# Kernel tuning notes

Measured on AMD Instinct MI355X. Metric: run time of the kernel, lower is better.

## Reference

```python
import jax, jax.numpy as jnp
import numpy as np
import math

H = 1024      # d_input / d_output channels
N = 64        # d_state (diagonal SSM size)
L = 2048      # kernel / sequence length
DT_MIN, DT_MAX = 0.001, 0.1
HIGH_STAB, LOW_STAB = -0.9, -0.8


def setup_inputs() -> dict:
    key = jax.random.key(0)
    k1, k2, k3, k4 = jax.random.split(key, 4)
    # log_dt ~ U[log(dt_min), log(dt_max)]
    log_dt = jax.random.uniform(k1, (H,), dtype=jnp.float32) \
        * (math.log(DT_MAX) - math.log(DT_MIN)) + math.log(DT_MIN)
    # C ~ complex normal, stored as real pairs (H, N, 2) like torch.view_as_real
    C = jax.random.normal(k2, (H, N, 2), dtype=jnp.float32)
    # Diagonal A: Re(A) uniform in [high_stability, low_stability] (stable),
    # Im(A) random; stored as real pairs (N, 2). A is a frozen buffer.
    a_re = jax.random.uniform(k3, (N,), dtype=jnp.float32) * (LOW_STAB - HIGH_STAB) + HIGH_STAB
    a_im = jax.random.normal(k4, (N,), dtype=jnp.float32) * math.pi
    A = jnp.stack([a_re, a_im], axis=-1)
    return {"log_dt": log_dt, "C": C, "A": A, "input_length": L}


def reference(log_dt, C, A, input_length):
    # log_dt: (H,) float32; C: (H,N,2) float32; A: (N,2) float32
    dt = jnp.exp(log_dt)                                   # (H,)
    Cc = (C[..., 0] + 1j * C[..., 1]).astype(jnp.complex64)  # (H, N)
    Ac = (A[..., 0] + 1j * A[..., 1]).astype(jnp.complex64)  # (N,)
    dtA = dt[:, None].astype(jnp.complex64) * Ac[None, :]  # (H, N)
    # Vandermonde-style kernel: exp(dtA * l) for l in [0, L)
    l = jnp.arange(input_length, dtype=jnp.float32).astype(jnp.complex64)  # (L,)
    Kexp = jnp.exp(dtA[:, :, None] * l[None, None, :])     # (H, N, L) complex64
    Cmod = Cc * (jnp.exp(dtA) - 1.0) / Ac                  # (H, N)
    K = 2.0 * jnp.einsum('hn,hnl->hl', Cmod, Kexp).real    # (H, L) float32
    return K
```

## Files before the change

### kernel.cpp

```cpp
#include <hip/hip_runtime.h>

#define H 1024
#define N 64
#define L 2048
#define TPB 256
#define KK (L / TPB)

#define INV2PI 0.15915494309189535f

__device__ __forceinline__ float fexp(float x) {
    return __expf(x);
}

__global__ void s4d_precomp(const float* __restrict__ log_dt,
                            const float* __restrict__ Cv,
                            const float* __restrict__ Av,
                            float4* __restrict__ P1,
                            float2* __restrict__ P2)
{
    int idx = blockIdx.x * blockDim.x + threadIdx.x;
    if (idx >= H * N) return;
    int h = idx >> 6;
    int n = idx & (N - 1);

    float dt = fexp(log_dt[h]);
    float ar = Av[2 * n], ai = Av[2 * n + 1];
    float dr = dt * ar, di = dt * ai;

    float mr  = fexp(dr);
    float rev = di * INV2PI;
    rev -= floorf(rev);
    float rr = mr * __builtin_amdgcn_cosf(rev);
    float ri = mr * __builtin_amdgcn_sinf(rev);

    float ms   = fexp(dr * (float)TPB);
    float revs = di * ((float)TPB * INV2PI);
    revs -= floorf(revs);
    float sr = ms * __builtin_amdgcn_cosf(revs);
    float si = ms * __builtin_amdgcn_sinf(revs);

    float cr = Cv[2 * idx], ci = Cv[2 * idx + 1];
    float er = rr - 1.0f, ei = ri;
    float tr = cr * er - ci * ei;
    float ti = cr * ei + ci * er;
    float inv = 2.0f / (ar * ar + ai * ai);
    float cmr = (tr * ar + ti * ai) * inv;
    float cmi = (ti * ar - tr * ai) * inv;

    P1[idx] = make_float4(dr, di, sr, si);
    P2[idx] = make_float2(cmr, cmi);
}

__global__ __launch_bounds__(TPB) void s4d_main(const float4* __restrict__ P1,
                                                const float2* __restrict__ P2,
                                                float* __restrict__ out)
{
    __shared__ float4 l1[N];
    __shared__ float2 l2[N];

    const int h = blockIdx.x;
    const int t = threadIdx.x;
    if (t < N) {
        l1[t] = P1[h * N + t];
        l2[t] = P2[h * N + t];
    }
    __syncthreads();

    float acc[KK];
#pragma unroll
    for (int k = 0; k < KK; ++k) acc[k] = 0.0f;

    const float tf = (float)t;

#pragma unroll 2
    for (int n = 0; n < N; ++n) {
        float4 a = l1[n];
        float2 c = l2[n];

        float m   = fexp(a.x * tf);
        float rev = (a.y * tf) * INV2PI;
        rev -= floorf(rev);
        float cs = __builtin_amdgcn_cosf(rev);
        float sn = __builtin_amdgcn_sinf(rev);
        float wre = m * (c.x * cs - c.y * sn);
        float wim = m * (c.x * sn + c.y * cs);

#pragma unroll
        for (int k = 0; k < KK; ++k) {
            acc[k] += wre;
            float nr = wre * a.z - wim * a.w;
            wim      = wre * a.w + wim * a.z;
            wre      = nr;
        }
    }

    float* o = out + h * L + t;
#pragma unroll
    for (int k = 0; k < KK; ++k) o[k * TPB] = acc[k];
}

extern "C" void kernel_launch(void* const* d_in, const int* in_sizes, int n_in,
                              void* d_out, int out_size, void* d_ws, size_t ws_size,
                              hipStream_t stream) {
    const float* log_dt = (const float*)d_in[0];
    const float* Cv     = (const float*)d_in[1];
    const float* Av     = (const float*)d_in[2];
    float* out          = (float*)d_out;

    float4* P1 = (float4*)d_ws;
    float2* P2 = (float2*)((char*)d_ws + (size_t)H * N * sizeof(float4));

    s4d_precomp<<<(H * N + 255) / 256, 256, 0, stream>>>(log_dt, Cv, Av, P1, P2);
    s4d_main<<<H, TPB, 0, stream>>>(P1, P2, out);
}
```

Measured before the change: 87.78 us.

## Fuse precompute into main kernel and use packed FP32 complex math

The separate precompute kernel is folded into the main kernel: the first 64 threads of each block compute the per-(h,n) decay, step and C-modulation terms directly into shared memory, which removes one launch and the workspace round trip. The inner complex recurrence now uses inline-asm v_pk_mul_f32/v_pk_fma_f32 and v_pk_add_f32 on two-wide float vectors, aiming to halve the VALU instruction count of the complex multiply-accumulate. The accumulator also carries an unused imaginary lane, which doubles accumulator registers and packed-add work. The 2π scaling is folded into the stored phase to save a multiply per step.

```diff
diff --git a/kernel.cpp b/kernel.cpp
--- a/kernel.cpp
+++ b/kernel.cpp
@@ -8,95 +8,99 @@
 
 #define INV2PI 0.15915494309189535f
 
-__device__ __forceinline__ float fexp(float x) {
-    return __expf(x);
+typedef float f32x2 __attribute__((ext_vector_type(2)));
+
+
+__device__ __forceinline__ f32x2 pk_add(f32x2 a, f32x2 b) {
+    f32x2 d;
+    asm("v_pk_add_f32 %0, %1, %2" : "=v"(d) : "v"(a), "v"(b));
+    return d;
 }
 
-__global__ void s4d_precomp(const float* __restrict__ log_dt,
-                            const float* __restrict__ Cv,
-                            const float* __restrict__ Av,
-                            float4* __restrict__ P1,
-                            float2* __restrict__ P2)
-{
-    int idx = blockIdx.x * blockDim.x + threadIdx.x;
-    if (idx >= H * N) return;
-    int h = idx >> 6;
-    int n = idx & (N - 1);
-
-    float dt = fexp(log_dt[h]);
-    float ar = Av[2 * n], ai = Av[2 * n + 1];
-    float dr = dt * ar, di = dt * ai;
-
-    float mr  = fexp(dr);
-    float rev = di * INV2PI;
-    rev -= floorf(rev);
-    float rr = mr * __builtin_amdgcn_cosf(rev);
-    float ri = mr * __builtin_amdgcn_sinf(rev);
-
-    float ms   = fexp(dr * (float)TPB);
-    float revs = di * ((float)TPB * INV2PI);
-    revs -= floorf(revs);
-    float sr = ms * __builtin_amdgcn_cosf(revs);
-    float si = ms * __builtin_amdgcn_sinf(revs);
-
-    float cr = Cv[2 * idx], ci = Cv[2 * idx + 1];
-    float er = rr - 1.0f, ei = ri;
-    float tr = cr * er - ci * ei;
-    float ti = cr * ei + ci * er;
-    float inv = 2.0f / (ar * ar + ai * ai);
-    float cmr = (tr * ar + ti * ai) * inv;
-    float cmi = (ti * ar - tr * ai) * inv;
-
-    P1[idx] = make_float4(dr, di, sr, si);
-    P2[idx] = make_float2(cmr, cmi);
+__device__ __forceinline__ f32x2 cmul(f32x2 w, f32x2 s) {
+    f32x2 t, r;
+    asm("v_pk_mul_f32 %0, %1, %2 op_sel_hi:[1,0]"
+        : "=v"(t) : "v"(w), "v"(s));
+    asm("v_pk_fma_f32 %0, %1, %2, %3 op_sel:[1,1,0] op_sel_hi:[0,1,1] neg_lo:[1,0,0]"
+        : "=v"(r) : "v"(w), "v"(s), "v"(t));
+    return r;
 }
 
-__global__ __launch_bounds__(TPB) void s4d_main(const float4* __restrict__ P1,
-                                                const float2* __restrict__ P2,
-                                                float* __restrict__ out)
+__global__ __launch_bounds__(TPB) void s4d_fused(const float* __restrict__ log_dt,
+                                                 const float* __restrict__ Cv,
+                                                 const float* __restrict__ Av,
+                                                 float* __restrict__ out)
 {
-    __shared__ float4 l1[N];
-    __shared__ float2 l2[N];
+    __shared__ float4 p1[N];
+    __shared__ f32x2 p2[N];
 
     const int h = blockIdx.x;
     const int t = threadIdx.x;
+
     if (t < N) {
-        l1[t] = P1[h * N + t];
-        l2[t] = P2[h * N + t];
+        float dt = __expf(log_dt[h]);
+        float2 a2 = ((const float2*)Av)[t];
+        float ar = a2.x, ai = a2.y;
+        float dr = dt * ar;
+        float direv = dt * ai * INV2PI;
+
+        float mr  = __expf(dr);
+        float rev = direv - floorf(direv);
+        float rr = mr * __builtin_amdgcn_cosf(rev);
+        float ri = mr * __builtin_amdgcn_sinf(rev);
+
+        float ms   = __expf(dr * (float)TPB);
+        float revs = direv * (float)TPB;
+        revs -= floorf(revs);
+        float sr = ms * __builtin_amdgcn_cosf(revs);
+        float si = ms * __builtin_amdgcn_sinf(revs);
+
+        float2 c2 = ((const float2*)Cv)[h * N + t];
+        float er = rr - 1.0f, ei = ri;
+        float tr = c2.x * er - c2.y * ei;
+        float ti = c2.x * ei + c2.y * er;
+        float inv = 2.0f / (ar * ar + ai * ai);
+        f32x2 cm;
+        cm.x = (tr * ar + ti * ai) * inv;
+        cm.y = (ti * ar - tr * ai) * inv;
+
+        p1[t] = make_float4(dr, direv, sr, si);
+        p2[t] = cm;
     }
     __syncthreads();
 
-    float acc[KK];
+    f32x2 acc[KK];
 #pragma unroll
-    for (int k = 0; k < KK; ++k) acc[k] = 0.0f;
+    for (int k = 0; k < KK; ++k) acc[k] = (f32x2)(0.0f);
 
     const float tf = (float)t;
 
 #pragma unroll 2
     for (int n = 0; n < N; ++n) {
-        float4 a = l1[n];
-        float2 c = l2[n];
+        float4 a   = p1[n];
+        f32x2 cmv  = p2[n];
 
-        float m   = fexp(a.x * tf);
-        float rev = (a.y * tf) * INV2PI;
+        float m   = __expf(a.x * tf);
+        float rev = a.y * tf;
         rev -= floorf(rev);
-        float cs = __builtin_amdgcn_cosf(rev);
-        float sn = __builtin_amdgcn_sinf(rev);
-        float wre = m * (c.x * cs - c.y * sn);
-        float wim = m * (c.x * sn + c.y * cs);
+        f32x2 e;
+        e.x = m * __builtin_amdgcn_cosf(rev);
+        e.y = m * __builtin_amdgcn_sinf(rev);
+        f32x2 w = cmul(e, cmv);
+
+        f32x2 s;
+        s.x = a.z; s.y = a.w;
 
 #pragma unroll
         for (int k = 0; k < KK; ++k) {
-            acc[k] += wre;
-            float nr = wre * a.z - wim * a.w;
-            wim      = wre * a.w + wim * a.z;
-            wre      = nr;
+            acc[k] = pk_add(acc[k], w);
+            w = cmul(w, s);
         }
     }
 
     float* o = out + h * L + t;
 #pragma unroll
-    for (int k = 0; k < KK; ++k) o[k * TPB] = acc[k];
+    for (int k = 0; k < KK; ++k) o[k * TPB] = acc[k].x;
 }
 
 extern "C" void kernel_launch(void* const* d_in, const int* in_sizes, int n_in,
@@ -107,9 +111,5 @@
     const float* Av     = (const float*)d_in[2];
     float* out          = (float*)d_out;
 
-    float4* P1 = (float4*)d_ws;
-    float2* P2 = (float2*)((char*)d_ws + (size_t)H * N * sizeof(float4));
-
-    s4d_precomp<<<(H * N + 255) / 256, 256, 0, stream>>>(log_dt, Cv, Av, P1, P2);
-    s4d_main<<<H, TPB, 0, stream>>>(P1, P2, out);
+    s4d_fused<<<H, TPB, 0, stream>>>(log_dt, Cv, Av, out);
 }
```

Result: faster. 79.69 us (-9.2%).
